# Kernel optimization log

Hardware: AMD Instinct MI355X
Metric: run time of the kernel (lower is better)

The kernel has to match this reference:

```python
import jax, jax.numpy as jnp
import numpy as np

B, NQ, NC1, NC2 = 2, 1024, 1024, 1024
QD = CD1 = CD2 = 1024
H, DH = 8, 64
INNER = H * DH          # 512
VD = 1024               # v_dim, split across heads -> 128 per head
VDH = VD // H


def setup_inputs() -> dict:
    key = jax.random.key(0)
    ks = jax.random.split(key, 18)
    f = lambda k, shape: jax.random.normal(k, shape, jnp.float32) * 0.02
    return {
        "x": f(ks[0], (B, NQ, QD)),
        "context": f(ks[1], (B, NC1, CD1)),
        "context2": f(ks[2], (B, NC2, CD2)),
        "mask1": jax.random.uniform(ks[3], (B, NQ, NC1)) > 0.1,
        "mask2": jax.random.uniform(ks[4], (B, NQ, NC2)) > 0.1,
        "Wq": f(ks[5], (QD, INNER)),  "bq": f(ks[6], (INNER,)),
        "Wk1": f(ks[7], (CD1, INNER)), "bk1": f(ks[8], (INNER,)),
        "Wv1": f(ks[9], (CD1, VD)),    "bv1": f(ks[10], (VD,)),
        "Wk2": f(ks[11], (CD2, INNER)), "bk2": f(ks[12], (INNER,)),
        "Wv2": f(ks[13], (CD2, VD)),    "bv2": f(ks[14], (VD,)),
        "Wo": f(ks[15], (VD, VD)),      "bo": f(ks[16], (VD,)),
    }


def _split_heads(t, d):
    # b n (h d) -> b h n d
    b, n, _ = t.shape
    return t.reshape(b, n, H, d).transpose(0, 2, 1, 3)


def reference(x, context, context2, mask1, mask2,
              Wq, bq, Wk1, bk1, Wv1, bv1, Wk2, bk2, Wv2, bv2, Wo, bo):
    scale = DH ** -0.5
    q = x @ Wq + bq
    k = jnp.concatenate([context @ Wk1 + bk1, context2 @ Wk2 + bk2], axis=1)
    v = jnp.concatenate([context @ Wv1 + bv1, context2 @ Wv2 + bv2], axis=1)

    qh = _split_heads(q, DH)   # [B,H,NQ,DH]
    kh = _split_heads(k, DH)   # [B,H,NC1+NC2,DH]
    vh = _split_heads(v, VDH)  # [B,H,NC1+NC2,VDH]

    sim = jnp.einsum('bhid,bhjd->bhij', qh, kh) * scale  # [B,H,NQ,J]
    mask = jnp.concatenate([mask1, mask2], axis=2)[:, None, :, :]  # [B,1,NQ,J]
    max_neg = -jnp.finfo(sim.dtype).max
    sim = jnp.where(mask, sim, max_neg)

    attn = jax.nn.softmax(sim, axis=-1)
    out = jnp.einsum('bhij,bhjd->bhid', attn, vh)          # [B,H,NQ,VDH]
    out = out.transpose(0, 2, 1, 3).reshape(B, NQ, VD)     # b n (h d)
    return out @ Wo + bo
```

## Files before the change

kernel.cpp:

```cpp
#include <hip/hip_runtime.h>
#include <math.h>

typedef short bf16x8 __attribute__((ext_vector_type(8)));
typedef float f32x4  __attribute__((ext_vector_type(4)));

__device__ __forceinline__ unsigned short f2bf(float f) {
    unsigned int u = __builtin_bit_cast(unsigned int, f);
    u += 0x7FFFu + ((u >> 16) & 1u);
    return (unsigned short)(u >> 16);
}
__device__ __forceinline__ float bf2f(unsigned short u) {
    return __builtin_bit_cast(float, (unsigned int)u << 16);
}

__device__ __forceinline__ void gld16(const unsigned short* g, unsigned short* l) {
    __builtin_amdgcn_global_load_lds(
        (const __attribute__((address_space(1))) void*)g,
        (__attribute__((address_space(3))) void*)l, 16, 0, 0);
}

__global__ __launch_bounds__(256) void prep(
    const float* __restrict__ x, const float* __restrict__ c1, const float* __restrict__ c2,
    const int* __restrict__ mask1, const int* __restrict__ mask2,
    const float* __restrict__ Wq, const float* __restrict__ Wk1, const float* __restrict__ Wk2,
    const float* __restrict__ Wv1, const float* __restrict__ Wv2, const float* __restrict__ Wo,
    unsigned short* __restrict__ xb, unsigned short* __restrict__ c1b, unsigned short* __restrict__ c2b,
    unsigned short* __restrict__ Wqt, unsigned short* __restrict__ Wk1t, unsigned short* __restrict__ Wk2t,
    unsigned short* __restrict__ Wv1t, unsigned short* __restrict__ Wv2t, unsigned short* __restrict__ Wot,
    unsigned long long* __restrict__ mpk)
{
    __shared__ float T[64][65];
    const int bid = blockIdx.x, t = threadIdx.x;

    if (bid < 3072) {
        const int z = bid >> 10;
        const float* a = z == 0 ? x : (z == 1 ? c1 : c2);
        unsigned short* o = z == 0 ? xb : (z == 1 ? c1b : c2b);
        size_t i = ((size_t)(bid & 1023) * 256 + t) * 8;
        float4 x0 = *(const float4*)&a[i];
        float4 x1 = *(const float4*)&a[i + 4];
        uint4 pk;
        pk.x = (unsigned)f2bf(x0.x) | ((unsigned)f2bf(x0.y) << 16);
        pk.y = (unsigned)f2bf(x0.z) | ((unsigned)f2bf(x0.w) << 16);
        pk.z = (unsigned)f2bf(x1.x) | ((unsigned)f2bf(x1.y) << 16);
        pk.w = (unsigned)f2bf(x1.z) | ((unsigned)f2bf(x1.w) << 16);
        *(uint4*)&o[i] = pk;
        return;
    }
    if (bid < 4224) {
        const float* W; unsigned short* O; int N, n0, k0; bool perm = false;
        if (bid < 3456) {
            int l = bid - 3072, z = l >> 7, rem = l & 127;
            W = z == 0 ? Wq : (z == 1 ? Wk1 : Wk2);
            O = z == 0 ? Wqt : (z == 1 ? Wk1t : Wk2t);
            N = 512; n0 = (rem & 7) << 6; k0 = (rem >> 3) << 6;
        } else {
            int l = bid - 3456, z = l >> 8, rem = l & 255;
            W = z == 0 ? Wv1 : (z == 1 ? Wv2 : Wo);
            O = z == 0 ? Wv1t : (z == 1 ? Wv2t : Wot);
            N = 1024; n0 = (rem & 15) << 6; k0 = (rem >> 4) << 6;
            perm = (z == 2);
        }
        #pragma unroll
        for (int i = 0; i < 4; i++) {
            int vi = t + (i << 8);
            int r = vi >> 4, c4 = (vi & 15) << 2;
            *(float4*)&T[r][c4] = *(const float4*)&W[(size_t)(k0 + r) * N + n0 + c4];
        }
        __syncthreads();
        #pragma unroll
        for (int i = 0; i < 4; i++) {
            int vi = t + (i << 8);
            int n = vi >> 4, k4 = (vi & 15) << 2;
            if (!perm) {
                uint2 pk;
                pk.x = (unsigned)f2bf(T[k4 + 0][n]) | ((unsigned)f2bf(T[k4 + 1][n]) << 16);
                pk.y = (unsigned)f2bf(T[k4 + 2][n]) | ((unsigned)f2bf(T[k4 + 3][n]) << 16);
                *(uint2*)&O[(size_t)(n0 + n) * 1024 + k0 + k4] = pk;
            } else {
                #pragma unroll
                for (int ii = 0; ii < 4; ii++) {
                    int k = k0 + k4 + ii, f = k & 127;
                    int kp = (k & ~127) | ((f & 15) << 3) | (f >> 4);
                    O[(size_t)(n0 + n) * 1024 + kp] = f2bf(T[k4 + ii][n]);
                }
            }
        }
        return;
    }
    {
        int wid = ((bid - 4224) << 2) + (t >> 6);
        int lane = t & 63;
        const int* m1 = mask1 + ((size_t)wid << 10);
        const int* m2 = mask2 + ((size_t)wid << 10);
        unsigned long long* o = mpk + ((size_t)wid << 5);
        #pragma unroll
        for (int win = 0; win < 16; win++) {
            unsigned long long bal = __ballot(m1[(win << 6) + lane] != 0);
            if (lane == 0) o[win] = bal;
        }
        #pragma unroll
        for (int win = 0; win < 16; win++) {
            unsigned long long bal = __ballot(m2[(win << 6) + lane] != 0);
            if (lane == 0) o[16 + win] = bal;
        }
    }
}

template<int NT>
__device__ __forceinline__ void gemm_core(
    const unsigned short* __restrict__ A,
    const unsigned short* __restrict__ Wt,
    int K, int gm0, int gn0,
    unsigned short (*As)[32], unsigned short (*Bs)[32],
    f32x4 (&acc)[4][NT / 32])
{
    constexpr int NS = NT / 32;
    const int t = threadIdx.x;
    const int lane = t & 63, w = t >> 6;
    const int wm = (w & 1) << 6, wn = (w >> 1) * (NT / 2);
    const int l15 = lane & 15, quad = lane >> 4;

    for (int k0 = 0; k0 < K; k0 += 32) {
        __syncthreads();
        #pragma unroll
        for (int i = 0; i < 2; i++) {
            int r0 = (i << 6) + (w << 4);
            int ra = r0 + (lane >> 2);
            int kc = (lane & 3) << 3;
            gld16(&A[(size_t)(gm0 + ra) * K + k0 + kc], &As[r0][0] + ((size_t)lane << 3));
        }
        #pragma unroll
        for (int i = 0; i < NT / 64; i++) {
            int r0 = (i << 6) + (w << 4);
            int ra = r0 + (lane >> 2);
            int kc = (lane & 3) << 3;
            gld16(&Wt[(size_t)(gn0 + ra) * K + k0 + kc], &Bs[r0][0] + ((size_t)lane << 3));
        }
        __syncthreads();
        bf16x8 af[4], bg[NS];
        #pragma unroll
        for (int i = 0; i < 4; i++)
            af[i] = *(const bf16x8*)&As[wm + (i << 4) + l15][quad << 3];
        #pragma unroll
        for (int j = 0; j < NS; j++)
            bg[j] = *(const bf16x8*)&Bs[wn + (j << 4) + l15][quad << 3];
        #pragma unroll
        for (int i = 0; i < 4; i++)
            #pragma unroll
            for (int j = 0; j < NS; j++)
                acc[i][j] = __builtin_amdgcn_mfma_f32_16x16x32_bf16(af[i], bg[j], acc[i][j], 0, 0, 0);
    }
}

__global__ __launch_bounds__(256) void proj_all(
    const unsigned short* __restrict__ xb, const unsigned short* __restrict__ c1b,
    const unsigned short* __restrict__ c2b,
    const unsigned short* __restrict__ Wqt, const unsigned short* __restrict__ Wk1t,
    const unsigned short* __restrict__ Wk2t, const unsigned short* __restrict__ Wv1t,
    const unsigned short* __restrict__ Wv2t,
    const float* __restrict__ bq, const float* __restrict__ bk1, const float* __restrict__ bk2,
    const float* __restrict__ bv1, const float* __restrict__ bv2,
    unsigned short* __restrict__ qbuf, unsigned short* __restrict__ khb,
    unsigned short* __restrict__ vhb)
{
    __shared__ unsigned short As[128][32];
    __shared__ unsigned short Bs[128][32];
    const int bid = blockIdx.x;
    int z, bx, by;
    if (bid < 192) { z = bid >> 6; int l = bid & 63; by = l >> 2; bx = l & 3; }
    else { int l = bid - 192; z = 3 + (l >> 7); l &= 127; by = l >> 3; bx = l & 7; }
    const unsigned short* A  = (z == 0) ? xb : (z == 1 || z == 3) ? c1b : c2b;
    const unsigned short* Wt = (z == 0) ? Wqt : (z == 1) ? Wk1t : (z == 2) ? Wk2t
                             : (z == 3) ? Wv1t : Wv2t;
    const float* bias = (z == 0) ? bq : (z == 1) ? bk1 : (z == 2) ? bk2
                      : (z == 3) ? bv1 : bv2;
    const int gm0 = by << 7, gn0 = bx << 7;

    f32x4 acc[4][4];
    #pragma unroll
    for (int i = 0; i < 4; i++)
        #pragma unroll
        for (int j = 0; j < 4; j++) acc[i][j] = (f32x4){0.f, 0.f, 0.f, 0.f};

    gemm_core<128>(A, Wt, 1024, gm0, gn0, As, Bs, acc);

    const int lane = threadIdx.x & 63, w = threadIdx.x >> 6;
    const int wm = (w & 1) << 6, wn = (w >> 1) << 6;
    const int l15 = lane & 15, quad = lane >> 4;
    float bb[4];
    #pragma unroll
    for (int j = 0; j < 4; j++) bb[j] = bias[gn0 + wn + (j << 4) + l15];

    if (z == 0) {
        #pragma unroll
        for (int i = 0; i < 4; i++) {
            int mb = gm0 + wm + (i << 4) + (quad << 2);
            #pragma unroll
            for (int p = 0; p < 4; p++)
                #pragma unroll
                for (int j = 0; j < 4; j++)
                    qbuf[(size_t)(mb + p) * 512 + gn0 + wn + (j << 4) + l15] = f2bf(acc[i][j][p] + bb[j]);
        }
    } else if (z < 3) {
        const int off = (z == 2) ? 1024 : 0;
        #pragma unroll
        for (int i = 0; i < 4; i++) {
            int mb = gm0 + wm + (i << 4) + (quad << 2);
            int b = mb >> 10;
            #pragma unroll
            for (int j = 0; j < 4; j++) {
                int n = gn0 + wn + (j << 4) + l15;
                int hh = n >> 6, d = n & 63;
                size_t hb = ((size_t)((b << 3) + hh) << 17);
                #pragma unroll
                for (int p = 0; p < 4; p++) {
                    int jrow = off + ((mb + p) & 1023);
                    khb[hb + ((size_t)jrow << 6) + ((((d >> 3) ^ (jrow & 7))) << 3) + (d & 7)]
                        = f2bf(acc[i][j][p] + bb[j]);
                }
            }
        }
    } else {
        const int off = (z == 3) ? 0 : 1024;
        #pragma unroll
        for (int i = 0; i < 4; i++) {
            int mb = gm0 + wm + (i << 4) + (quad << 2);
            int b = mb >> 10;
            int jj = (mb & 1023) + off;
            #pragma unroll
            for (int j = 0; j < 4; j++) {
                int n = gn0 + wn + (j << 4) + l15;
                int hh = n >> 7, f = n & 127;
                size_t base = ((size_t)((b << 3) + hh) << 18) + ((size_t)f << 11);
                int jpos = (jj & ~63) | ((((jj >> 3) & 7) ^ (f & 7)) << 3) | (jj & 7);
                unsigned long long pk = 0;
                #pragma unroll
                for (int p = 0; p < 4; p++)
                    pk |= (unsigned long long)f2bf(acc[i][j][p] + bb[j]) << (16 * p);
                *(unsigned long long*)&vhb[base + jpos] = pk;
            }
        }
    }
}

__global__ __launch_bounds__(256) void gemm_out(
    const unsigned short* __restrict__ abuf, const unsigned short* __restrict__ Wot,
    const float* __restrict__ bo, float* __restrict__ out)
{
    __shared__ unsigned short As[128][32];
    __shared__ unsigned short Bs[64][32];
    const int gm0 = blockIdx.y << 7, gn0 = blockIdx.x << 6;

    f32x4 acc[4][2];
    #pragma unroll
    for (int i = 0; i < 4; i++)
        #pragma unroll
        for (int j = 0; j < 2; j++) acc[i][j] = (f32x4){0.f, 0.f, 0.f, 0.f};

    gemm_core<64>(abuf, Wot, 1024, gm0, gn0, As, Bs, acc);

    const int lane = threadIdx.x & 63, w = threadIdx.x >> 6;
    const int wm = (w & 1) << 6, wn = (w >> 1) << 5;
    const int l15 = lane & 15, quad = lane >> 4;
    float bb[2];
    #pragma unroll
    for (int j = 0; j < 2; j++) bb[j] = bo[gn0 + wn + (j << 4) + l15];
    #pragma unroll
    for (int i = 0; i < 4; i++) {
        int mb = gm0 + wm + (i << 4) + (quad << 2);
        #pragma unroll
        for (int p = 0; p < 4; p++)
            #pragma unroll
            for (int j = 0; j < 2; j++)
                out[(size_t)(mb + p) * 1024 + gn0 + wn + (j << 4) + l15] = acc[i][j][p] + bb[j];
    }
}

__global__ __launch_bounds__(256) void attn_mfma(
    const unsigned short* __restrict__ qbuf, const unsigned short* __restrict__ khb,
    const unsigned short* __restrict__ vhb, const unsigned long long* __restrict__ mpk,
    unsigned short* __restrict__ Opart, float* __restrict__ ml)
{
    __shared__ unsigned short Ks[64 * 64];
    __shared__ unsigned short VsT[128 * 64];
    __shared__ unsigned short Ps[64 * 64];

    const int t = threadIdx.x;
    const int bid = blockIdx.x;
    const int hs = bid >> 8, r = bid & 255;
    const int h = r & 7, qt = (r >> 3) & 15, b = r >> 7;
    const int q0 = qt << 6;
    const int lane = t & 63, w = t >> 6, l15 = lane & 15, quad = lane >> 4;
    const int v7 = l15 & 7;

    const unsigned short* qrow = qbuf + (((size_t)(b << 10) + q0 + (w << 4) + l15) << 9) + (h << 6);
    const bf16x8 aq0 = *(const bf16x8*)&qrow[quad << 3];
    const bf16x8 aq1 = *(const bf16x8*)&qrow[32 + (quad << 3)];

    f32x4 acc[8];
    #pragma unroll
    for (int ct = 0; ct < 8; ct++) acc[ct] = (f32x4){0.f, 0.f, 0.f, 0.f};
    float m_l = -3.0e38f, l_l = 0.f;

    const unsigned short* kh = khb + ((size_t)((b << 3) + h) << 17);
    const unsigned short* vh = vhb + ((size_t)((b << 3) + h) << 18);
    const unsigned long long* mrow = mpk + (((size_t)(b << 10) + q0 + (w << 4) + l15) << 5) + (hs << 3);
    const int prow = ((w << 4) + l15) << 6;

    for (int jt = 0; jt < 8; jt++) {
        const int j0 = (hs << 9) + (jt << 6);
        __syncthreads();
        {
            const unsigned short* kg = kh + ((size_t)j0 << 6);
            int o = (w << 10) + (lane << 3);
            gld16(kg + o, Ks + o);
            gld16(kg + o + 512, Ks + o + 512);
        }
        #pragma unroll
        for (int it = 0; it < 4; it++) {
            int f0 = (w << 5) + (it << 3);
            gld16(vh + ((size_t)(f0 + (lane >> 3)) << 11) + j0 + ((lane & 7) << 3),
                  VsT + (f0 << 6) + (lane << 3));
        }
        __syncthreads();

        const unsigned long long mw = mrow[jt];

        f32x4 s[4];
        #pragma unroll
        for (int n = 0; n < 4; n++) {
            int rowk = (n << 4) + l15;
            bf16x8 bk0 = *(const bf16x8*)&Ks[(rowk << 6) + ((quad ^ v7) << 3)];
            bf16x8 bk1 = *(const bf16x8*)&Ks[(rowk << 6) + (((quad + 4) ^ v7) << 3)];
            s[n] = (f32x4){0.f, 0.f, 0.f, 0.f};
            s[n] = __builtin_amdgcn_mfma_f32_16x16x32_bf16(bk0, aq0, s[n], 0, 0, 0);
            s[n] = __builtin_amdgcn_mfma_f32_16x16x32_bf16(bk1, aq1, s[n], 0, 0, 0);
        }
        #pragma unroll
        for (int n = 0; n < 4; n++)
            #pragma unroll
            for (int p = 0; p < 4; p++) {
                float sv = s[n][p] * 0.125f;
                s[n][p] = ((mw >> ((n << 4) + (quad << 2) + p)) & 1ull) ? sv : -3.0e38f;
            }

        float mt = s[0][0];
        #pragma unroll
        for (int n = 0; n < 4; n++)
            #pragma unroll
            for (int p = 0; p < 4; p++) mt = fmaxf(mt, s[n][p]);
        mt = fmaxf(mt, __shfl_xor(mt, 16, 64));
        mt = fmaxf(mt, __shfl_xor(mt, 32, 64));
        float mn = fmaxf(m_l, mt);
        float ls = 0.f;
        #pragma unroll
        for (int n = 0; n < 4; n++) {
            float e0 = __expf(s[n][0] - mn), e1 = __expf(s[n][1] - mn);
            float e2 = __expf(s[n][2] - mn), e3 = __expf(s[n][3] - mn);
            ls += (e0 + e1) + (e2 + e3);
            unsigned long long pk = (unsigned long long)f2bf(e0)
                | ((unsigned long long)f2bf(e1) << 16)
                | ((unsigned long long)f2bf(e2) << 32)
                | ((unsigned long long)f2bf(e3) << 48);
            int mblk = ((n << 1) + (quad >> 1)) ^ v7;
            *(unsigned long long*)&Ps[prow + (mblk << 3) + ((quad & 1) << 2)] = pk;
        }
        ls += __shfl_xor(ls, 16, 64);
        ls += __shfl_xor(ls, 32, 64);
        float al = __expf(m_l - mn);
        l_l = l_l * al + ls;
        m_l = mn;

        float ar[4];
        #pragma unroll
        for (int p = 0; p < 4; p++)
            ar[p] = __shfl(al, (lane & 48) | ((quad << 2) + p), 64);
        #pragma unroll
        for (int ct = 0; ct < 8; ct++)
            #pragma unroll
            for (int p = 0; p < 4; p++) acc[ct][p] *= ar[p];

        bf16x8 ap[2];
        #pragma unroll
        for (int win = 0; win < 2; win++) {
            int mblk = ((win << 2) + quad) ^ v7;
            ap[win] = *(const bf16x8*)&Ps[prow + (mblk << 3)];
        }
        #pragma unroll
        for (int ct = 0; ct < 8; ct++) {
            int f = (ct << 4) + l15;
            #pragma unroll
            for (int win = 0; win < 2; win++) {
                int c = (win << 2) + quad;
                bf16x8 bv = *(const bf16x8*)&VsT[(f << 6) + ((c ^ v7) << 3)];
                acc[ct] = __builtin_amdgcn_mfma_f32_16x16x32_bf16(ap[win], bv, acc[ct], 0, 0, 0);
            }
        }
    }

    #pragma unroll
    for (int p = 0; p < 4; p++) {
        int q = q0 + (w << 4) + (quad << 2) + p;
        size_t idx = ((size_t)hs << 14) + ((size_t)((b << 3) + h) << 10) + q;
        uint4 pk;
        pk.x = (unsigned)f2bf(acc[0][p]) | ((unsigned)f2bf(acc[1][p]) << 16);
        pk.y = (unsigned)f2bf(acc[2][p]) | ((unsigned)f2bf(acc[3][p]) << 16);
        pk.z = (unsigned)f2bf(acc[4][p]) | ((unsigned)f2bf(acc[5][p]) << 16);
        pk.w = (unsigned)f2bf(acc[6][p]) | ((unsigned)f2bf(acc[7][p]) << 16);
        *(uint4*)&Opart[(idx << 7) + (l15 << 3)] = pk;
    }
    if (quad == 0) {
        int q = q0 + (w << 4) + l15;
        size_t idx = ((size_t)hs << 14) + ((size_t)((b << 3) + h) << 10) + q;
        ml[(idx << 1) + 0] = m_l;
        ml[(idx << 1) + 1] = l_l;
    }
}

__global__ __launch_bounds__(256) void attn_combine(
    const unsigned short* __restrict__ Opart, const float* __restrict__ ml,
    unsigned short* __restrict__ abuf)
{
    int id = (blockIdx.x << 8) + threadIdx.x;
    int bhq = id >> 5, c = id & 31;
    float2 m0 = ((const float2*)ml)[bhq];
    float2 m1 = ((const float2*)ml)[16384 + bhq];
    float2 m2 = ((const float2*)ml)[32768 + bhq];
    float2 m3 = ((const float2*)ml)[49152 + bhq];
    float M = fmaxf(fmaxf(m0.x, m1.x), fmaxf(m2.x, m3.x));
    float a0 = __expf(m0.x - M), a1 = __expf(m1.x - M);
    float a2 = __expf(m2.x - M), a3 = __expf(m3.x - M);
    float inv = 1.0f / (m0.y * a0 + m1.y * a1 + m2.y * a2 + m3.y * a3);
    a0 *= inv; a1 *= inv; a2 *= inv; a3 *= inv;
    float o[4] = {0.f, 0.f, 0.f, 0.f};
    float as[4] = {a0, a1, a2, a3};
    #pragma unroll
    for (int s = 0; s < 4; s++) {
        uint2 v = *(const uint2*)&Opart[((size_t)(s * 16384 + bhq) << 7) + (c << 2)];
        o[0] += as[s] * bf2f((unsigned short)(v.x & 0xFFFF));
        o[1] += as[s] * bf2f((unsigned short)(v.x >> 16));
        o[2] += as[s] * bf2f((unsigned short)(v.y & 0xFFFF));
        o[3] += as[s] * bf2f((unsigned short)(v.y >> 16));
    }
    int b = bhq >> 13, hh = (bhq >> 10) & 7, q = bhq & 1023;
    unsigned long long pk = (unsigned long long)f2bf(o[0])
        | ((unsigned long long)f2bf(o[1]) << 16)
        | ((unsigned long long)f2bf(o[2]) << 32)
        | ((unsigned long long)f2bf(o[3]) << 48);
    *(unsigned long long*)&abuf[((size_t)((b << 10) + q) << 10) + (hh << 7) + (c << 2)] = pk;
}

extern "C" void kernel_launch(void* const* d_in, const int* in_sizes, int n_in,
                              void* d_out, int out_size, void* d_ws, size_t ws_size,
                              hipStream_t stream)
{
    const float* x        = (const float*)d_in[0];
    const float* context  = (const float*)d_in[1];
    const float* context2 = (const float*)d_in[2];
    const int*   mask1    = (const int*)d_in[3];
    const int*   mask2    = (const int*)d_in[4];
    const float* Wq  = (const float*)d_in[5];
    const float* bq  = (const float*)d_in[6];
    const float* Wk1 = (const float*)d_in[7];
    const float* bk1 = (const float*)d_in[8];
    const float* Wv1 = (const float*)d_in[9];
    const float* bv1 = (const float*)d_in[10];
    const float* Wk2 = (const float*)d_in[11];
    const float* bk2 = (const float*)d_in[12];
    const float* Wv2 = (const float*)d_in[13];
    const float* bv2 = (const float*)d_in[14];
    const float* Wo  = (const float*)d_in[15];
    const float* bo  = (const float*)d_in[16];
    float* out = (float*)d_out;

    char* W = (char*)d_ws;
    unsigned short* Wot  = (unsigned short*)(W);
    unsigned short* xb   = (unsigned short*)(W + (2ull  << 20));
    unsigned short* c1b  = (unsigned short*)(W + (6ull  << 20));
    unsigned short* c2b  = (unsigned short*)(W + (10ull << 20));
    unsigned short* Wqt  = (unsigned short*)(W + (14ull << 20));
    unsigned short* Wk1t = (unsigned short*)(W + (15ull << 20));
    unsigned short* Wk2t = (unsigned short*)(W + (16ull << 20));
    unsigned short* Wv1t = (unsigned short*)(W + (17ull << 20));
    unsigned short* Wv2t = (unsigned short*)(W + (19ull << 20));
    unsigned short* qbuf = (unsigned short*)(W + (21ull << 20));
    unsigned short* khb  = (unsigned short*)(W + (23ull << 20));
    unsigned short* vhb  = (unsigned short*)(W + (27ull << 20));
    unsigned long long* mpk = (unsigned long long*)(W + (35ull << 20));
    float*          mlb  = (float*)(W + (35ull << 20) + (1ull << 19));
    unsigned short* Opart = (unsigned short*)(W + (2ull << 20));
    unsigned short* abuf  = (unsigned short*)(W + (19ull << 20));

    prep<<<dim3(4736), 256, 0, stream>>>(x, context, context2, mask1, mask2,
                                         Wq, Wk1, Wk2, Wv1, Wv2, Wo,
                                         xb, c1b, c2b, Wqt, Wk1t, Wk2t, Wv1t, Wv2t, Wot, mpk);
    proj_all<<<dim3(448), 256, 0, stream>>>(xb, c1b, c2b, Wqt, Wk1t, Wk2t, Wv1t, Wv2t,
                                            bq, bk1, bk2, bv1, bv2, qbuf, khb, vhb);
    attn_mfma<<<dim3(1024), 256, 0, stream>>>(qbuf, khb, vhb, mpk, Opart, mlb);
    attn_combine<<<dim3(2048), 256, 0, stream>>>(Opart, mlb, abuf);
    gemm_out<<<dim3(16, 16), 256, 0, stream>>>(abuf, Wot, bo, out);
}
```

Baseline: 218.0 us.

## Double query rows per attention block and stage K/V projection stores through LDS

The attention kernel now gives each wave two 16-row query slices (128 queries per block, half the blocks), so every K and V tile loaded into LDS feeds twice as many MFMAs. The softmax scale is folded into the Q projection epilogue, which removes the per-score multiply. The K and V projection epilogues write results into a padded shared tile first and then emit 16-byte coalesced stores in the swizzled head layout, replacing scattered 2- and 8-byte global writes. Costs are higher register pressure in attention (two accumulator sets) and fewer blocks to fill the GPU.

```diff
diff --git a/kernel.cpp b/kernel.cpp
--- a/kernel.cpp
+++ b/kernel.cpp
@@ -164,8 +164,11 @@
     unsigned short* __restrict__ qbuf, unsigned short* __restrict__ khb,
     unsigned short* __restrict__ vhb)
 {
-    __shared__ unsigned short As[128][32];
-    __shared__ unsigned short Bs[128][32];
+    __shared__ unsigned short smem[17408];
+    unsigned short (*As)[32] = (unsigned short(*)[32])smem;
+    unsigned short (*Bs)[32] = (unsigned short(*)[32])(smem + 4096);
+    unsigned short* Ts = smem;
+
     const int bid = blockIdx.x;
     int z, bx, by;
     if (bid < 192) { z = bid >> 6; int l = bid & 63; by = l >> 2; bx = l & 3; }
@@ -185,7 +188,8 @@
 
     gemm_core<128>(A, Wt, 1024, gm0, gn0, As, Bs, acc);
 
-    const int lane = threadIdx.x & 63, w = threadIdx.x >> 6;
+    const int t = threadIdx.x;
+    const int lane = t & 63, w = t >> 6;
     const int wm = (w & 1) << 6, wn = (w >> 1) << 6;
     const int l15 = lane & 15, quad = lane >> 4;
     float bb[4];
@@ -200,46 +204,62 @@
             for (int p = 0; p < 4; p++)
                 #pragma unroll
                 for (int j = 0; j < 4; j++)
-                    qbuf[(size_t)(mb + p) * 512 + gn0 + wn + (j << 4) + l15] = f2bf(acc[i][j][p] + bb[j]);
-        }
-    } else if (z < 3) {
-        const int off = (z == 2) ? 1024 : 0;
+                    qbuf[(size_t)(mb + p) * 512 + gn0 + wn + (j << 4) + l15]
+                        = f2bf((acc[i][j][p] + bb[j]) * 0.125f);
+        }
+        return;
+    }
+
+    __syncthreads();
+    const int b = gm0 >> 10;
+    if (z < 3) {
+        const int jb = ((z == 2) ? 1024 : 0) + (gm0 & 1023);
         #pragma unroll
         for (int i = 0; i < 4; i++) {
-            int mb = gm0 + wm + (i << 4) + (quad << 2);
-            int b = mb >> 10;
+            int jl0 = wm + (i << 4) + (quad << 2);
             #pragma unroll
             for (int j = 0; j < 4; j++) {
-                int n = gn0 + wn + (j << 4) + l15;
-                int hh = n >> 6, d = n & 63;
-                size_t hb = ((size_t)((b << 3) + hh) << 17);
-                #pragma unroll
-                for (int p = 0; p < 4; p++) {
-                    int jrow = off + ((mb + p) & 1023);
-                    khb[hb + ((size_t)jrow << 6) + ((((d >> 3) ^ (jrow & 7))) << 3) + (d & 7)]
-                        = f2bf(acc[i][j][p] + bb[j]);
-                }
-            }
+                int n = wn + (j << 4) + l15;
+                #pragma unroll
+                for (int p = 0; p < 4; p++)
+                    Ts[(jl0 + p) * 136 + n] = f2bf(acc[i][j][p] + bb[j]);
+            }
+        }
+        __syncthreads();
+        #pragma unroll
+        for (int rr = 0; rr < 8; rr++) {
+            int row = (rr << 4) + (t >> 4), cd = t & 15;
+            uint4 v = *(const uint4*)&Ts[row * 136 + (cd << 3)];
+            int jg = jb + row;
+            int hcol = (gn0 >> 6) + (cd >> 3);
+            size_t hb = ((size_t)((b << 3) + hcol) << 17);
+            *(uint4*)&khb[hb + ((size_t)jg << 6) + ((((cd & 7) ^ (jg & 7))) << 3)] = v;
         }
     } else {
-        const int off = (z == 3) ? 0 : 1024;
+        const int jb = ((z == 3) ? 0 : 1024) + (gm0 & 1023);
         #pragma unroll
         for (int i = 0; i < 4; i++) {
-            int mb = gm0 + wm + (i << 4) + (quad << 2);
-            int b = mb >> 10;
-            int jj = (mb & 1023) + off;
+            int jl0 = wm + (i << 4) + (quad << 2);
             #pragma unroll
             for (int j = 0; j < 4; j++) {
-                int n = gn0 + wn + (j << 4) + l15;
-                int hh = n >> 7, f = n & 127;
-                size_t base = ((size_t)((b << 3) + hh) << 18) + ((size_t)f << 11);
-                int jpos = (jj & ~63) | ((((jj >> 3) & 7) ^ (f & 7)) << 3) | (jj & 7);
+                int n = wn + (j << 4) + l15;
                 unsigned long long pk = 0;
                 #pragma unroll
                 for (int p = 0; p < 4; p++)
                     pk |= (unsigned long long)f2bf(acc[i][j][p] + bb[j]) << (16 * p);
-                *(unsigned long long*)&vhb[base + jpos] = pk;
-            }
+                *(unsigned long long*)&Ts[n * 136 + jl0] = pk;
+            }
+        }
+        __syncthreads();
+        const int hv = gn0 >> 7;
+        size_t hbase = ((size_t)((b << 3) + hv) << 18);
+        #pragma unroll
+        for (int rr = 0; rr < 8; rr++) {
+            int f = (rr << 4) + (t >> 4), cj = t & 15;
+            uint4 v = *(const uint4*)&Ts[f * 136 + (cj << 3)];
+            int jj = jb + (cj << 3);
+            int jpos = (jj & ~63) | ((((jj >> 3) & 7) ^ (f & 7)) << 3);
+            *(uint4*)&vhb[hbase + ((size_t)f << 11) + jpos] = v;
         }
     }
 }
@@ -284,29 +304,40 @@
 {
     __shared__ unsigned short Ks[64 * 64];
     __shared__ unsigned short VsT[128 * 64];
-    __shared__ unsigned short Ps[64 * 64];
+    __shared__ unsigned short Ps[128 * 64];
 
     const int t = threadIdx.x;
     const int bid = blockIdx.x;
-    const int hs = bid >> 8, r = bid & 255;
-    const int h = r & 7, qt = (r >> 3) & 15, b = r >> 7;
-    const int q0 = qt << 6;
+    const int h = bid & 7, b = (bid >> 3) & 1, qt = (bid >> 4) & 7, hs = bid >> 7;
+    const int Q0 = qt << 7;
     const int lane = t & 63, w = t >> 6, l15 = lane & 15, quad = lane >> 4;
     const int v7 = l15 & 7;
 
-    const unsigned short* qrow = qbuf + (((size_t)(b << 10) + q0 + (w << 4) + l15) << 9) + (h << 6);
-    const bf16x8 aq0 = *(const bf16x8*)&qrow[quad << 3];
-    const bf16x8 aq1 = *(const bf16x8*)&qrow[32 + (quad << 3)];
-
-    f32x4 acc[8];
-    #pragma unroll
-    for (int ct = 0; ct < 8; ct++) acc[ct] = (f32x4){0.f, 0.f, 0.f, 0.f};
-    float m_l = -3.0e38f, l_l = 0.f;
+    bf16x8 aq[2][2];
+    #pragma unroll
+    for (int qs = 0; qs < 2; qs++) {
+        const unsigned short* qrow =
+            qbuf + (((size_t)(b << 10) + Q0 + (w << 5) + (qs << 4) + l15) << 9) + (h << 6);
+        aq[qs][0] = *(const bf16x8*)&qrow[quad << 3];
+        aq[qs][1] = *(const bf16x8*)&qrow[32 + (quad << 3)];
+    }
+
+    f32x4 acc[2][8];
+    #pragma unroll
+    for (int qs = 0; qs < 2; qs++)
+        #pragma unroll
+        for (int ct = 0; ct < 8; ct++) acc[qs][ct] = (f32x4){0.f, 0.f, 0.f, 0.f};
+    float m_l[2] = {-3.0e38f, -3.0e38f}, l_l[2] = {0.f, 0.f};
 
     const unsigned short* kh = khb + ((size_t)((b << 3) + h) << 17);
     const unsigned short* vh = vhb + ((size_t)((b << 3) + h) << 18);
-    const unsigned long long* mrow = mpk + (((size_t)(b << 10) + q0 + (w << 4) + l15) << 5) + (hs << 3);
-    const int prow = ((w << 4) + l15) << 6;
+    const unsigned long long* mrow[2];
+    int prow[2];
+    #pragma unroll
+    for (int qs = 0; qs < 2; qs++) {
+        mrow[qs] = mpk + (((size_t)(b << 10) + Q0 + (w << 5) + (qs << 4) + l15) << 5) + (hs << 3);
+        prow[qs] = ((w << 5) + (qs << 4) + l15) << 6;
+    }
 
     for (int jt = 0; jt < 8; jt++) {
         const int j0 = (hs << 9) + (jt << 6);
@@ -325,68 +356,76 @@
         }
         __syncthreads();
 
-        const unsigned long long mw = mrow[jt];
-
-        f32x4 s[4];
+        f32x4 s[2][4];
         #pragma unroll
         for (int n = 0; n < 4; n++) {
             int rowk = (n << 4) + l15;
             bf16x8 bk0 = *(const bf16x8*)&Ks[(rowk << 6) + ((quad ^ v7) << 3)];
             bf16x8 bk1 = *(const bf16x8*)&Ks[(rowk << 6) + (((quad + 4) ^ v7) << 3)];
-            s[n] = (f32x4){0.f, 0.f, 0.f, 0.f};
-            s[n] = __builtin_amdgcn_mfma_f32_16x16x32_bf16(bk0, aq0, s[n], 0, 0, 0);
-            s[n] = __builtin_amdgcn_mfma_f32_16x16x32_bf16(bk1, aq1, s[n], 0, 0, 0);
-        }
-        #pragma unroll
-        for (int n = 0; n < 4; n++)
-            #pragma unroll
-            for (int p = 0; p < 4; p++) {
-                float sv = s[n][p] * 0.125f;
-                s[n][p] = ((mw >> ((n << 4) + (quad << 2) + p)) & 1ull) ? sv : -3.0e38f;
-            }
-
-        float mt = s[0][0];
-        #pragma unroll
-        for (int n = 0; n < 4; n++)
-            #pragma unroll
-            for (int p = 0; p < 4; p++) mt = fmaxf(mt, s[n][p]);
-        mt = fmaxf(mt, __shfl_xor(mt, 16, 64));
-        mt = fmaxf(mt, __shfl_xor(mt, 32, 64));
-        float mn = fmaxf(m_l, mt);
-        float ls = 0.f;
-        #pragma unroll
-        for (int n = 0; n < 4; n++) {
-            float e0 = __expf(s[n][0] - mn), e1 = __expf(s[n][1] - mn);
-            float e2 = __expf(s[n][2] - mn), e3 = __expf(s[n][3] - mn);
-            ls += (e0 + e1) + (e2 + e3);
-            unsigned long long pk = (unsigned long long)f2bf(e0)
-                | ((unsigned long long)f2bf(e1) << 16)
-                | ((unsigned long long)f2bf(e2) << 32)
-                | ((unsigned long long)f2bf(e3) << 48);
-            int mblk = ((n << 1) + (quad >> 1)) ^ v7;
-            *(unsigned long long*)&Ps[prow + (mblk << 3) + ((quad & 1) << 2)] = pk;
-        }
-        ls += __shfl_xor(ls, 16, 64);
-        ls += __shfl_xor(ls, 32, 64);
-        float al = __expf(m_l - mn);
-        l_l = l_l * al + ls;
-        m_l = mn;
-
-        float ar[4];
-        #pragma unroll
-        for (int p = 0; p < 4; p++)
-            ar[p] = __shfl(al, (lane & 48) | ((quad << 2) + p), 64);
-        #pragma unroll
-        for (int ct = 0; ct < 8; ct++)
-            #pragma unroll
-            for (int p = 0; p < 4; p++) acc[ct][p] *= ar[p];
-
-        bf16x8 ap[2];
-        #pragma unroll
-        for (int win = 0; win < 2; win++) {
-            int mblk = ((win << 2) + quad) ^ v7;
-            ap[win] = *(const bf16x8*)&Ps[prow + (mblk << 3)];
-        }
+            #pragma unroll
+            for (int qs = 0; qs < 2; qs++) {
+                f32x4 z = (n == 0) ? (f32x4){0.f, 0.f, 0.f, 0.f} : s[qs][n];
+                (void)z;
+                s[qs][n] = (f32x4){0.f, 0.f, 0.f, 0.f};
+                s[qs][n] = __builtin_amdgcn_mfma_f32_16x16x32_bf16(bk0, aq[qs][0], s[qs][n], 0, 0, 0);
+                s[qs][n] = __builtin_amdgcn_mfma_f32_16x16x32_bf16(bk1, aq[qs][1], s[qs][n], 0, 0, 0);
+            }
+        }
+
+        float ar[2][4];
+        #pragma unroll
+        for (int qs = 0; qs < 2; qs++) {
+            const unsigned long long mw = mrow[qs][jt];
+            #pragma unroll
+            for (int n = 0; n < 4; n++)
+                #pragma unroll
+                for (int p = 0; p < 4; p++)
+                    s[qs][n][p] = ((mw >> ((n << 4) + (quad << 2) + p)) & 1ull)
+                                ? s[qs][n][p] : -3.0e38f;
+
+            float mt = s[qs][0][0];
+            #pragma unroll
+            for (int n = 0; n < 4; n++)
+                #pragma unroll
+                for (int p = 0; p < 4; p++) mt = fmaxf(mt, s[qs][n][p]);
+            mt = fmaxf(mt, __shfl_xor(mt, 16, 64));
+            mt = fmaxf(mt, __shfl_xor(mt, 32, 64));
+            float mn = fmaxf(m_l[qs], mt);
+            float ls = 0.f;
+            #pragma unroll
+            for (int n = 0; n < 4; n++) {
+                float e0 = __expf(s[qs][n][0] - mn), e1 = __expf(s[qs][n][1] - mn);
+                float e2 = __expf(s[qs][n][2] - mn), e3 = __expf(s[qs][n][3] - mn);
+                ls += (e0 + e1) + (e2 + e3);
+                unsigned long long pk = (unsigned long long)f2bf(e0)
+                    | ((unsigned long long)f2bf(e1) << 16)
+                    | ((unsigned long long)f2bf(e2) << 32)
+                    | ((unsigned long long)f2bf(e3) << 48);
+                int mblk = ((n << 1) + (quad >> 1)) ^ v7;
+                *(unsigned long long*)&Ps[prow[qs] + (mblk << 3) + ((quad & 1) << 2)] = pk;
+            }
+            ls += __shfl_xor(ls, 16, 64);
+            ls += __shfl_xor(ls, 32, 64);
+            float al = __expf(m_l[qs] - mn);
+            l_l[qs] = l_l[qs] * al + ls;
+            m_l[qs] = mn;
+            #pragma unroll
+            for (int p = 0; p < 4; p++)
+                ar[qs][p] = __shfl(al, (lane & 48) | ((quad << 2) + p), 64);
+            #pragma unroll
+            for (int ct = 0; ct < 8; ct++)
+                #pragma unroll
+                for (int p = 0; p < 4; p++) acc[qs][ct][p] *= ar[qs][p];
+        }
+
+        bf16x8 ap[2][2];
+        #pragma unroll
+        for (int qs = 0; qs < 2; qs++)
+            #pragma unroll
+            for (int win = 0; win < 2; win++) {
+                int mblk = ((win << 2) + quad) ^ v7;
+                ap[qs][win] = *(const bf16x8*)&Ps[prow[qs] + (mblk << 3)];
+            }
         #pragma unroll
         for (int ct = 0; ct < 8; ct++) {
             int f = (ct << 4) + l15;
@@ -394,27 +433,31 @@
             for (int win = 0; win < 2; win++) {
                 int c = (win << 2) + quad;
                 bf16x8 bv = *(const bf16x8*)&VsT[(f << 6) + ((c ^ v7) << 3)];
-                acc[ct] = __builtin_amdgcn_mfma_f32_16x16x32_bf16(ap[win], bv, acc[ct], 0, 0, 0);
-            }
-        }
-    }
-
-    #pragma unroll
-    for (int p = 0; p < 4; p++) {
-        int q = q0 + (w << 4) + (quad << 2) + p;
-        size_t idx = ((size_t)hs << 14) + ((size_t)((b << 3) + h) << 10) + q;
-        uint4 pk;
-        pk.x = (unsigned)f2bf(acc[0][p]) | ((unsigned)f2bf(acc[1][p]) << 16);
-        pk.y = (unsigned)f2bf(acc[2][p]) | ((unsigned)f2bf(acc[3][p]) << 16);
-        pk.z = (unsigned)f2bf(acc[4][p]) | ((unsigned)f2bf(acc[5][p]) << 16);
-        pk.w = (unsigned)f2bf(acc[6][p]) | ((unsigned)f2bf(acc[7][p]) << 16);
-        *(uint4*)&Opart[(idx << 7) + (l15 << 3)] = pk;
-    }
-    if (quad == 0) {
-        int q = q0 + (w << 4) + l15;
-        size_t idx = ((size_t)hs << 14) + ((size_t)((b << 3) + h) << 10) + q;
-        ml[(idx << 1) + 0] = m_l;
-        ml[(idx << 1) + 1] = l_l;
+                acc[0][ct] = __builtin_amdgcn_mfma_f32_16x16x32_bf16(ap[0][win], bv, acc[0][ct], 0, 0, 0);
+                acc[1][ct] = __builtin_amdgcn_mfma_f32_16x16x32_bf16(ap[1][win], bv, acc[1][ct], 0, 0, 0);
+            }
+        }
+    }
+
+    #pragma unroll
+    for (int qs = 0; qs < 2; qs++) {
+        #pragma unroll
+        for (int p = 0; p < 4; p++) {
+            int q = Q0 + (w << 5) + (qs << 4) + (quad << 2) + p;
+            size_t idx = ((size_t)hs << 14) + ((size_t)((b << 3) + h) << 10) + q;
+            uint4 pk;
+            pk.x = (unsigned)f2bf(acc[qs][0][p]) | ((unsigned)f2bf(acc[qs][1][p]) << 16);
+            pk.y = (unsigned)f2bf(acc[qs][2][p]) | ((unsigned)f2bf(acc[qs][3][p]) << 16);
+            pk.z = (unsigned)f2bf(acc[qs][4][p]) | ((unsigned)f2bf(acc[qs][5][p]) << 16);
+            pk.w = (unsigned)f2bf(acc[qs][6][p]) | ((unsigned)f2bf(acc[qs][7][p]) << 16);
+            *(uint4*)&Opart[(idx << 7) + (l15 << 3)] = pk;
+        }
+        if (quad == 0) {
+            int q = Q0 + (w << 5) + (qs << 4) + l15;
+            size_t idx = ((size_t)hs << 14) + ((size_t)((b << 3) + h) << 10) + q;
+            ml[(idx << 1) + 0] = m_l[qs];
+            ml[(idx << 1) + 1] = l_l[qs];
+        }
     }
 }
 
@@ -497,7 +540,7 @@
                                          xb, c1b, c2b, Wqt, Wk1t, Wk2t, Wv1t, Wv2t, Wot, mpk);
     proj_all<<<dim3(448), 256, 0, stream>>>(xb, c1b, c2b, Wqt, Wk1t, Wk2t, Wv1t, Wv2t,
                                             bq, bk1, bk2, bv1, bv2, qbuf, khb, vhb);
-    attn_mfma<<<dim3(1024), 256, 0, stream>>>(qbuf, khb, vhb, mpk, Opart, mlb);
+    attn_mfma<<<dim3(512), 256, 0, stream>>>(qbuf, khb, vhb, mpk, Opart, mlb);
     attn_combine<<<dim3(2048), 256, 0, stream>>>(Opart, mlb, abuf);
     gemm_out<<<dim3(16, 16), 256, 0, stream>>>(abuf, Wot, bo, out);
 }
```

Measured after the change: 228.4 us. 1.05x slower.

## Stage K/V projection epilogue through LDS and fold softmax scale into Q

Applied to the files above, without the earlier changes.

The K and V projection epilogues now write tiles into shared memory first, then emit 16-byte coalesced stores in the swizzled head layout instead of scattered 2-byte and 8-byte writes. The softmax scale times log2(e) is folded into Q at projection time, so attention drops the per-score multiply and uses native exp2. P is packed to bf16 by truncation via a byte-permute instead of round-to-nearest. The cost is an extra LDS round trip and barrier in the projection kernel, plus slightly lower precision from truncating P.

```diff
diff --git a/kernel.cpp b/kernel.cpp
--- a/kernel.cpp
+++ b/kernel.cpp
@@ -12,12 +12,18 @@
 __device__ __forceinline__ float bf2f(unsigned short u) {
     return __builtin_bit_cast(float, (unsigned int)u << 16);
 }
+__device__ __forceinline__ unsigned pktrunc(float hi, float lo) {
+    return __builtin_amdgcn_perm(__builtin_bit_cast(unsigned, hi),
+                                 __builtin_bit_cast(unsigned, lo), 0x07060302u);
+}
 
 __device__ __forceinline__ void gld16(const unsigned short* g, unsigned short* l) {
     __builtin_amdgcn_global_load_lds(
         (const __attribute__((address_space(1))) void*)g,
         (__attribute__((address_space(3))) void*)l, 16, 0, 0);
 }
+
+#define QSCALE 0.18033688011112042f
 
 __global__ __launch_bounds__(256) void prep(
     const float* __restrict__ x, const float* __restrict__ c1, const float* __restrict__ c2,
@@ -164,8 +170,11 @@
     unsigned short* __restrict__ qbuf, unsigned short* __restrict__ khb,
     unsigned short* __restrict__ vhb)
 {
-    __shared__ unsigned short As[128][32];
-    __shared__ unsigned short Bs[128][32];
+    __shared__ unsigned short smem[17408];
+    unsigned short (*As)[32] = (unsigned short(*)[32])smem;
+    unsigned short (*Bs)[32] = (unsigned short(*)[32])(smem + 4096);
+    unsigned short* Ts = smem;
+
     const int bid = blockIdx.x;
     int z, bx, by;
     if (bid < 192) { z = bid >> 6; int l = bid & 63; by = l >> 2; bx = l & 3; }
@@ -185,7 +194,8 @@
 
     gemm_core<128>(A, Wt, 1024, gm0, gn0, As, Bs, acc);
 
-    const int lane = threadIdx.x & 63, w = threadIdx.x >> 6;
+    const int t = threadIdx.x;
+    const int lane = t & 63, w = t >> 6;
     const int wm = (w & 1) << 6, wn = (w >> 1) << 6;
     const int l15 = lane & 15, quad = lane >> 4;
     float bb[4];
@@ -200,46 +210,62 @@
             for (int p = 0; p < 4; p++)
                 #pragma unroll
                 for (int j = 0; j < 4; j++)
-                    qbuf[(size_t)(mb + p) * 512 + gn0 + wn + (j << 4) + l15] = f2bf(acc[i][j][p] + bb[j]);
-        }
-    } else if (z < 3) {
-        const int off = (z == 2) ? 1024 : 0;
+                    qbuf[(size_t)(mb + p) * 512 + gn0 + wn + (j << 4) + l15]
+                        = f2bf((acc[i][j][p] + bb[j]) * QSCALE);
+        }
+        return;
+    }
+
+    __syncthreads();
+    const int b = gm0 >> 10;
+    if (z < 3) {
+        const int jb = ((z == 2) ? 1024 : 0) + (gm0 & 1023);
         #pragma unroll
         for (int i = 0; i < 4; i++) {
-            int mb = gm0 + wm + (i << 4) + (quad << 2);
-            int b = mb >> 10;
+            int jl0 = wm + (i << 4) + (quad << 2);
             #pragma unroll
             for (int j = 0; j < 4; j++) {
-                int n = gn0 + wn + (j << 4) + l15;
-                int hh = n >> 6, d = n & 63;
-                size_t hb = ((size_t)((b << 3) + hh) << 17);
+                int n = wn + (j << 4) + l15;
                 #pragma unroll
-                for (int p = 0; p < 4; p++) {
-                    int jrow = off + ((mb + p) & 1023);
-                    khb[hb + ((size_t)jrow << 6) + ((((d >> 3) ^ (jrow & 7))) << 3) + (d & 7)]
-                        = f2bf(acc[i][j][p] + bb[j]);
-                }
+                for (int p = 0; p < 4; p++)
+                    Ts[(jl0 + p) * 136 + n] = f2bf(acc[i][j][p] + bb[j]);
             }
         }
+        __syncthreads();
+        #pragma unroll
+        for (int rr = 0; rr < 8; rr++) {
+            int row = (rr << 4) + (t >> 4), cd = t & 15;
+            uint4 v = *(const uint4*)&Ts[row * 136 + (cd << 3)];
+            int jg = jb + row;
+            int hcol = (gn0 >> 6) + (cd >> 3);
+            size_t hb = ((size_t)((b << 3) + hcol) << 17);
+            *(uint4*)&khb[hb + ((size_t)jg << 6) + ((((cd & 7) ^ (jg & 7))) << 3)] = v;
+        }
     } else {
-        const int off = (z == 3) ? 0 : 1024;
+        const int jb = ((z == 3) ? 0 : 1024) + (gm0 & 1023);
         #pragma unroll
         for (int i = 0; i < 4; i++) {
-            int mb = gm0 + wm + (i << 4) + (quad << 2);
-            int b = mb >> 10;
-            int jj = (mb & 1023) + off;
+            int jl0 = wm + (i << 4) + (quad << 2);
             #pragma unroll
             for (int j = 0; j < 4; j++) {
-                int n = gn0 + wn + (j << 4) + l15;
-                int hh = n >> 7, f = n & 127;
-                size_t base = ((size_t)((b << 3) + hh) << 18) + ((size_t)f << 11);
-                int jpos = (jj & ~63) | ((((jj >> 3) & 7) ^ (f & 7)) << 3) | (jj & 7);
+                int n = wn + (j << 4) + l15;
                 unsigned long long pk = 0;
                 #pragma unroll
                 for (int p = 0; p < 4; p++)
                     pk |= (unsigned long long)f2bf(acc[i][j][p] + bb[j]) << (16 * p);
-                *(unsigned long long*)&vhb[base + jpos] = pk;
+                *(unsigned long long*)&Ts[n * 136 + jl0] = pk;
             }
+        }
+        __syncthreads();
+        const int hv = gn0 >> 7;
+        size_t hbase = ((size_t)((b << 3) + hv) << 18);
+        #pragma unroll
+        for (int rr = 0; rr < 8; rr++) {
+            int f = (rr << 4) + (t >> 4), cj = t & 15;
+            uint4 v = *(const uint4*)&Ts[f * 136 + (cj << 3)];
+            int jj = jb + (cj << 3);
+            int jpos = (jj & ~63) | ((((jj >> 3) & 7) ^ (f & 7)) << 3);
+            *(uint4*)&vhb[hbase + ((size_t)f << 11) + jpos] = v;
         }
     }
 }
@@ -340,10 +366,8 @@
         #pragma unroll
         for (int n = 0; n < 4; n++)
             #pragma unroll
-            for (int p = 0; p < 4; p++) {
-                float sv = s[n][p] * 0.125f;
-                s[n][p] = ((mw >> ((n << 4) + (quad << 2) + p)) & 1ull) ? sv : -3.0e38f;
-            }
+            for (int p = 0; p < 4; p++)
+                s[n][p] = ((mw >> ((n << 4) + (quad << 2) + p)) & 1ull) ? s[n][p] : -3.0e38f;
 
         float mt = s[0][0];
         #pragma unroll
@@ -356,19 +380,20 @@
         float ls = 0.f;
         #pragma unroll
         for (int n = 0; n < 4; n++) {
-            float e0 = __expf(s[n][0] - mn), e1 = __expf(s[n][1] - mn);
-            float e2 = __expf(s[n][2] - mn), e3 = __expf(s[n][3] - mn);
+            float e0 = __builtin_amdgcn_exp2f(s[n][0] - mn);
+            float e1 = __builtin_amdgcn_exp2f(s[n][1] - mn);
+            float e2 = __builtin_amdgcn_exp2f(s[n][2] - mn);
+            float e3 = __builtin_amdgcn_exp2f(s[n][3] - mn);
             ls += (e0 + e1) + (e2 + e3);
-            unsigned long long pk = (unsigned long long)f2bf(e0)
-                | ((unsigned long long)f2bf(e1) << 16)
-                | ((unsigned long long)f2bf(e2) << 32)
-                | ((unsigned long long)f2bf(e3) << 48);
+            uint2 pk;
+            pk.x = pktrunc(e1, e0);
+            pk.y = pktrunc(e3, e2);
             int mblk = ((n << 1) + (quad >> 1)) ^ v7;
-            *(unsigned long long*)&Ps[prow + (mblk << 3) + ((quad & 1) << 2)] = pk;
+            *(uint2*)&Ps[prow + (mblk << 3) + ((quad & 1) << 2)] = pk;
         }
         ls += __shfl_xor(ls, 16, 64);
         ls += __shfl_xor(ls, 32, 64);
-        float al = __expf(m_l - mn);
+        float al = __builtin_amdgcn_exp2f(m_l - mn);
         l_l = l_l * al + ls;
         m_l = mn;
 
@@ -429,8 +454,8 @@
     float2 m2 = ((const float2*)ml)[32768 + bhq];
     float2 m3 = ((const float2*)ml)[49152 + bhq];
     float M = fmaxf(fmaxf(m0.x, m1.x), fmaxf(m2.x, m3.x));
-    float a0 = __expf(m0.x - M), a1 = __expf(m1.x - M);
-    float a2 = __expf(m2.x - M), a3 = __expf(m3.x - M);
+    float a0 = __builtin_amdgcn_exp2f(m0.x - M), a1 = __builtin_amdgcn_exp2f(m1.x - M);
+    float a2 = __builtin_amdgcn_exp2f(m2.x - M), a3 = __builtin_amdgcn_exp2f(m3.x - M);
     float inv = 1.0f / (m0.y * a0 + m1.y * a1 + m2.y * a2 + m3.y * a3);
     a0 *= inv; a1 *= inv; a2 *= inv; a3 *= inv;
     float o[4] = {0.f, 0.f, 0.f, 0.f};
```

Measured after the change: 219.9 us. Within noise of the previous version (+0.9%).
